# Kernel tuning notes

Hardware: AMD Instinct MI355X
Metric: run time of the kernel (lower is better)

Reference implementation:

```python
import jax, jax.numpy as jnp
import numpy as np

EPS = 1e-05


def layer_norm(x, a, b):
    m = jnp.mean(x, axis=-1, keepdims=True)
    v = jnp.var(x, axis=-1, keepdims=True)
    return a * (x - m) / jnp.sqrt(v + EPS) + b


def setup_inputs() -> dict:
    key = jax.random.key(0)
    ks = jax.random.split(key, 16)
    b, n, d, h = 1, 384, 128, 128
    s = 1.0 / np.sqrt(d)
    inp = {
        "x": jax.random.normal(ks[0], (b, n, n, d), dtype=jnp.float32),
        "norm_a": jnp.ones((d,), jnp.float32),
        "norm_b": jnp.zeros((d,), jnp.float32),
        "Wl": jax.random.normal(ks[1], (d, h), jnp.float32) * s,
        "bl": jnp.zeros((h,), jnp.float32),
        "Wr": jax.random.normal(ks[2], (d, h), jnp.float32) * s,
        "br": jnp.zeros((h,), jnp.float32),
        "Wlg": jax.random.normal(ks[3], (d, h), jnp.float32) * s,
        "blg": jnp.ones((h,), jnp.float32),
        "Wrg": jax.random.normal(ks[4], (d, h), jnp.float32) * s,
        "brg": jnp.ones((h,), jnp.float32),
        "Wog": jax.random.normal(ks[5], (d, h), jnp.float32) * s,
        "bog": jnp.ones((h,), jnp.float32),
        "on_a": jnp.ones((h,), jnp.float32),
        "on_b": jnp.zeros((h,), jnp.float32),
        "Wo": jax.random.normal(ks[6], (h, d), jnp.float32) * s,
        "bo": jnp.zeros((d,), jnp.float32),
    }
    return inp


def reference(x, norm_a, norm_b, Wl, bl, Wr, br, Wlg, blg, Wrg, brg, Wog, bog, on_a, on_b, Wo, bo):
    n = x.shape[1]
    xn = layer_norm(x, norm_a, norm_b)
    left = (xn @ Wl + bl) * jax.nn.sigmoid(xn @ Wlg + blg)
    right = (xn @ Wr + br) * jax.nn.sigmoid(xn @ Wrg + brg)
    out_gate = jax.nn.sigmoid(xn @ Wog + bog)
    # ingoing mix: out[b,i,j,d] = sum_k left[b,k,j,d] * right[b,k,i,d], in fp32
    out = jnp.einsum('bkjd,bkid->bijd', left.astype(jnp.float32), right.astype(jnp.float32)) / n
    out = out.astype(x.dtype)
    out = layer_norm(out, on_a, on_b) * out_gate
    return out @ Wo + bo
```

## Files before the change

kernel.cpp:

```cpp
#include <hip/hip_runtime.h>
#include <hip/hip_bf16.h>

#define NN 384
#define DD 128
#define MM (NN*NN)

typedef __attribute__((ext_vector_type(8))) short short8;
typedef __attribute__((ext_vector_type(4))) float f32x4;

__device__ __forceinline__ unsigned short f2bf(float f){
  unsigned u = __float_as_uint(f);
  u += 0x7fffu + ((u >> 16) & 1u);
  return (unsigned short)(u >> 16);
}
__device__ __forceinline__ float bf2f(unsigned short u){
  return __uint_as_float(((unsigned)u) << 16);
}
__device__ __forceinline__ float sigm(float x){
  return 1.0f / (1.0f + __expf(-x));
}
__device__ __forceinline__ unsigned cvtpk(float lo, float hi){
  unsigned r;
  asm("v_cvt_pk_bf16_f32 %0, %1, %2" : "=v"(r) : "v"(lo), "v"(hi));
  return r;
}
__device__ __forceinline__ f32x4 mfma16(short8 a, short8 b, f32x4 c){
  return __builtin_amdgcn_mfma_f32_16x16x32_bf16(a, b, c, 0, 0, 0);
}
__device__ __forceinline__ void gll16(const void* g, void* l){
  __builtin_amdgcn_global_load_lds(
      (const __attribute__((address_space(1))) unsigned int*)g,
      (__attribute__((address_space(3))) unsigned int*)l, 16, 0, 0);
}

__global__ void k_prep(const float* __restrict__ Wl, const float* __restrict__ Wlg,
                       const float* __restrict__ Wr, const float* __restrict__ Wrg,
                       const float* __restrict__ Wog, const float* __restrict__ Wo,
                       unsigned short* __restrict__ Wcat, unsigned short* __restrict__ Wot){
  int n = blockIdx.x;
  if(n < 640){
    const float* src; int col;
    if(n < 128){ src = Wl;  col = n; }
    else if(n < 256){ src = Wlg; col = n-128; }
    else if(n < 384){ src = Wr;  col = n-256; }
    else if(n < 512){ src = Wrg; col = n-384; }
    else            { src = Wog; col = n-512; }
    for(int k = threadIdx.x; k < 128; k += 64)
      Wcat[n*128 + k] = f2bf(src[k*128 + col]);
  } else {
    int c = n - 640;
    for(int k = threadIdx.x; k < 128; k += 64)
      Wot[c*128 + k] = f2bf(Wo[k*128 + c]);
  }
}

__global__ __launch_bounds__(256) void k_ln_x(const float* __restrict__ x,
    const float* __restrict__ na, const float* __restrict__ nb,
    unsigned short* __restrict__ xn){
  int wid = threadIdx.x >> 6, lane = threadIdx.x & 63;
  long r = (long)blockIdx.x*4 + wid;
  float2 v = *(const float2*)(x + r*DD + lane*2);
  float s  = v.x + v.y;
  float sq = v.x*v.x + v.y*v.y;
  #pragma unroll
  for(int m = 32; m >= 1; m >>= 1){ s += __shfl_xor(s, m); sq += __shfl_xor(sq, m); }
  float mean = s  * (1.0f/128.0f);
  float var  = sq * (1.0f/128.0f) - mean*mean;
  float rstd = rsqrtf(var + 1e-5f);
  float2 a = *(const float2*)(na + lane*2);
  float2 b = *(const float2*)(nb + lane*2);
  unsigned pk = (unsigned)f2bf(a.x*(v.x-mean)*rstd + b.x)
              | ((unsigned)f2bf(a.y*(v.y-mean)*rstd + b.y) << 16);
  *(unsigned*)(xn + r*DD + lane*2) = pk;
}

__global__ __launch_bounds__(256, 4) void k_proj(
    const unsigned short* __restrict__ xn, const unsigned short* __restrict__ Wcat,
    const float* __restrict__ bl, const float* __restrict__ blg,
    const float* __restrict__ br, const float* __restrict__ brg,
    unsigned short* __restrict__ Lt, unsigned short* __restrict__ Rt){
  __shared__ char lds[2][16384];
  const int tid = threadIdx.x;
  const int wid = tid >> 6, lane = tid & 63;
  const int lrow = lane & 15, lgrp = lane >> 4;
  const int b = blockIdx.x;
  const int f = b / 288;
  const int w = b % 288;

  const int ws = wid >> 1;
  const int wd = wid & 1;
  const int d  = f*32 + wd*16 + lrow;

  short8 bv[4], bg[4];
  #pragma unroll
  for(int ks = 0; ks < 4; ++ks){
    bv[ks] = *(const short8*)(Wcat + (ws*256 + d)*DD + ks*32 + lgrp*8);
    bg[ks] = *(const short8*)(Wcat + (ws*256 + 128 + d)*DD + ks*32 + lgrp*8);
  }
  const float b0v = (ws ? br  : bl )[d];
  const float b1v = (ws ? brg : blg)[d];
  const float sc  = ws ? 1.0f : (1.0f/384.0f);
  unsigned short* const base = (ws ? Rt : Lt) + (long)d*MM;

  auto stage = [&](int buf, int v){
    int j = v/6, kb = v%6;
    int rsub = lane >> 4, c = lane & 15;
    #pragma unroll
    for(int p = 0; p < 4; ++p){
      int r0 = p*16 + wid*4;
      int r = r0 + rsub;
      gll16(xn + ((long)(kb*64 + r)*NN + j)*DD + (c ^ (r & 7))*8, &lds[buf][r0*256]);
    }
  };

  stage(0, w*8);
  __syncthreads();
  int cur = 0;
  for(int i = 0; i < 8; ++i){
    int v = w*8 + i;
    if(i < 7) stage(cur^1, v+1);

    f32x4 zero = {0.f,0.f,0.f,0.f};
    f32x4 acc[4][2];
    #pragma unroll
    for(int a1=0;a1<4;++a1){ acc[a1][0] = zero; acc[a1][1] = zero; }

    #pragma unroll
    for(int ks = 0; ks < 4; ++ks){
      #pragma unroll
      for(int fr = 0; fr < 4; ++fr){
        int r = fr*16 + lrow;
        short8 af = *(const short8*)(&lds[cur][r*256 + (((ks*4+lgrp)*16) ^ ((r&7)<<4))]);
        acc[fr][0] = mfma16(af, bv[ks], acc[fr][0]);
        acc[fr][1] = mfma16(af, bg[ks], acc[fr][1]);
      }
    }

    int j = v/6, kb = v%6;
    unsigned short* dst = base + (long)j*NN + kb*64;
    #pragma unroll
    for(int fr = 0; fr < 4; ++fr){
      float v0 = (acc[fr][0][0] + b0v)*sigm(acc[fr][1][0] + b1v)*sc;
      float v1 = (acc[fr][0][1] + b0v)*sigm(acc[fr][1][1] + b1v)*sc;
      float v2 = (acc[fr][0][2] + b0v)*sigm(acc[fr][1][2] + b1v)*sc;
      float v3 = (acc[fr][0][3] + b0v)*sigm(acc[fr][1][3] + b1v)*sc;
      uint2 pk; pk.x = cvtpk(v0, v1); pk.y = cvtpk(v2, v3);
      *(uint2*)(dst + fr*16 + lgrp*4) = pk;
    }
    __syncthreads();
    cur ^= 1;
  }
}

__global__ __launch_bounds__(256) void k_einsum(
    const unsigned short* __restrict__ Rt, const unsigned short* __restrict__ Lt,
    unsigned short* __restrict__ mid){
  __shared__ char lds[65536];
  const int b = blockIdx.x;
  const int xcd = b & 7, slot = b >> 3;
  const int d = (slot/9)*8 + xcd;
  const int t = slot % 9;
  const int it = t/3, jt = t%3;
  const int i0 = it*128, j0 = jt*128;
  const unsigned short* Abase = Lt + (long)d*MM;
  const unsigned short* Bbase = Rt + (long)d*MM;
  const int wid = threadIdx.x >> 6, lane = threadIdx.x & 63;
  const int wr = wid >> 1, wc = wid & 1;
  const int lrow = lane & 15, lgrp = lane >> 4;

  auto stage = [&](int buf, int kt){
    int k = kt*64;
    int c = lane & 7;
    #pragma unroll
    for(int t8 = 0; t8 < 8; ++t8){
      int rr = wid*64 + t8*8 + (lane >> 3);
      int r = rr & 127;
      const unsigned short* src = (rr < 128) ? (Abase + (long)(j0+r)*NN + k)
                                             : (Bbase + (long)(i0+r)*NN + k);
      gll16(src + (c ^ (r & 7))*8, &lds[buf*32768 + (wid*64 + t8*8)*128]);
    }
  };

  f32x4 zero = {0.f,0.f,0.f,0.f};
  f32x4 acc[4][4];
  #pragma unroll
  for(int a1 = 0; a1 < 4; ++a1)
    #pragma unroll
    for(int a2 = 0; a2 < 4; ++a2) acc[a1][a2] = zero;

  stage(0, 0);
  __syncthreads();
  for(int kt = 0; kt < 6; ++kt){
    int cur = kt & 1;
    if(kt < 5) stage(cur ^ 1, kt + 1);
    const int base = cur*32768;
    #pragma unroll
    for(int ks = 0; ks < 2; ++ks){
      short8 af[4], bf[4];
      #pragma unroll
      for(int f = 0; f < 4; ++f){
        int rj = wr*64 + f*16 + lrow;
        af[f] = *(const short8*)(&lds[base + rj*128 + (((ks*4+lgrp)*16) ^ ((rj & 7) << 4))]);
        int ri = wc*64 + f*16 + lrow;
        bf[f] = *(const short8*)(&lds[base + 16384 + ri*128 + (((ks*4+lgrp)*16) ^ ((ri & 7) << 4))]);
      }
      #pragma unroll
      for(int fj = 0; fj < 4; ++fj)
        #pragma unroll
        for(int fi = 0; fi < 4; ++fi)
          acc[fj][fi] = mfma16(af[fj], bf[fi], acc[fj][fi]);
    }
    __syncthreads();
  }

  #pragma unroll
  for(int fj = 0; fj < 4; ++fj){
    int j = j0 + wr*64 + fj*16 + lgrp*4;
    #pragma unroll
    for(int fi = 0; fi < 4; ++fi){
      int i = i0 + wc*64 + fi*16 + lrow;
      uint2 pk;
      pk.x = cvtpk(acc[fj][fi][0], acc[fj][fi][1]);
      pk.y = cvtpk(acc[fj][fi][2], acc[fj][fi][3]);
      *(uint2*)(mid + (long)d*MM + (long)i*NN + j) = pk;
    }
  }
}

__global__ __launch_bounds__(256) void k_final(
    const unsigned short* __restrict__ mid, const unsigned short* __restrict__ xn,
    const unsigned short* __restrict__ Wcat,
    const float* __restrict__ bog,
    const float* __restrict__ ona, const float* __restrict__ onb,
    const unsigned short* __restrict__ Wot, const float* __restrict__ bo,
    float* __restrict__ out){
  __shared__ unsigned short midt[64][144];
  __shared__ char slds[16384];
  __shared__ char glds[16384];
  const int tid = threadIdx.x;
  const int wid = tid >> 6, lane = tid & 63;
  const int lrow = lane & 15, lgrp = lane >> 4;
  const int i = blockIdx.y;
  const int j0 = blockIdx.x*64;

  {
    int rsub = lane >> 4, c = lane & 15;
    #pragma unroll
    for(int p = 0; p < 4; ++p){
      int r0 = p*16 + wid*4;
      int r = r0 + rsub;
      gll16(xn + ((long)i*NN + j0 + r)*DD + (c ^ (r & 7))*8, &slds[r0*256]);
    }
  }
  const int wc = wid;
  short8 ag[2][4];
  #pragma unroll
  for(int cf = 0; cf < 2; ++cf)
    #pragma unroll
    for(int ks = 0; ks < 4; ++ks)
      ag[cf][ks] = *(const short8*)(Wcat + (512 + wc*32 + cf*16 + lrow)*DD + ks*32 + lgrp*8);

  {
    int jp = tid & 15, dr = tid >> 4;
    #pragma unroll
    for(int pass = 0; pass < 8; ++pass){
      int dd = pass*16 + dr;
      uint2 v = *(const uint2*)(mid + (long)dd*MM + (long)i*NN + j0 + jp*4);
      midt[jp*4+0][dd] = (unsigned short)(v.x & 0xffffu);
      midt[jp*4+1][dd] = (unsigned short)(v.x >> 16);
      midt[jp*4+2][dd] = (unsigned short)(v.y & 0xffffu);
      midt[jp*4+3][dd] = (unsigned short)(v.y >> 16);
    }
  }
  __syncthreads();

  {
    f32x4 zero = {0.f,0.f,0.f,0.f};
    f32x4 accg[2][4];
    #pragma unroll
    for(int a1=0;a1<2;++a1)
      #pragma unroll
      for(int a2=0;a2<4;++a2) accg[a1][a2] = zero;
    #pragma unroll
    for(int ks = 0; ks < 4; ++ks){
      short8 bx[4];
      #pragma unroll
      for(int mf = 0; mf < 4; ++mf){
        int r = mf*16 + lrow;
        bx[mf] = *(const short8*)(&slds[r*256 + (((ks*4+lgrp)*16) ^ ((r&7)<<4))]);
      }
      #pragma unroll
      for(int cf = 0; cf < 2; ++cf)
        #pragma unroll
        for(int mf = 0; mf < 4; ++mf)
          accg[cf][mf] = mfma16(ag[cf][ks], bx[mf], accg[cf][mf]);
    }
    #pragma unroll
    for(int cf = 0; cf < 2; ++cf){
      int c0 = wc*32 + cf*16 + lgrp*4;
      float4 b4 = *(const float4*)(bog + c0);
      #pragma unroll
      for(int mf = 0; mf < 4; ++mf){
        int rr = mf*16 + lrow;
        uint2 pk;
        pk.x = cvtpk(sigm(accg[cf][mf][0] + b4.x), sigm(accg[cf][mf][1] + b4.y));
        pk.y = cvtpk(sigm(accg[cf][mf][2] + b4.z), sigm(accg[cf][mf][3] + b4.w));
        *(uint2*)(&glds[rr*256 + ((c0*2) ^ ((rr&7)<<4))]) = pk;
      }
    }
  }
  __syncthreads();

  {
    int j = tid >> 2, s = tid & 3;
    float vals[32];
    float sum = 0.f, sq = 0.f;
    #pragma unroll
    for(int o8 = 0; o8 < 4; ++o8){
      short8 h = *(const short8*)(&midt[j][s*32 + o8*8]);
      #pragma unroll
      for(int q = 0; q < 8; ++q){
        float vq = bf2f((unsigned short)h[q]);
        vals[o8*8+q] = vq; sum += vq; sq += vq*vq;
      }
    }
    #pragma unroll
    for(int m = 1; m < 4; m <<= 1){ sum += __shfl_xor(sum, m); sq += __shfl_xor(sq, m); }
    float mean = sum*(1.f/128.f);
    float var  = sq *(1.f/128.f) - mean*mean;
    float rstd = rsqrtf(var + 1e-5f);
    #pragma unroll
    for(int o = 0; o < 32; o += 4){
      int dd = s*32 + o;
      uint2 gv = *(const uint2*)(&glds[j*256 + ((dd*2) ^ ((j&7)<<4))]);
      float g0 = bf2f((unsigned short)(gv.x & 0xffffu));
      float g1 = bf2f((unsigned short)(gv.x >> 16));
      float g2 = bf2f((unsigned short)(gv.y & 0xffffu));
      float g3 = bf2f((unsigned short)(gv.y >> 16));
      float4 a4 = *(const float4*)(ona + dd);
      float4 b4 = *(const float4*)(onb + dd);
      float v0 = (a4.x*(vals[o]  -mean)*rstd + b4.x)*g0;
      float v1 = (a4.y*(vals[o+1]-mean)*rstd + b4.y)*g1;
      float v2 = (a4.z*(vals[o+2]-mean)*rstd + b4.z)*g2;
      float v3 = (a4.w*(vals[o+3]-mean)*rstd + b4.w)*g3;
      uint2 pk; pk.x = cvtpk(v0, v1); pk.y = cvtpk(v2, v3);
      *(uint2*)(&slds[j*256 + ((dd*2) ^ ((j&7)<<4))]) = pk;
    }
  }
  __syncthreads();

  {
    f32x4 zero = {0.f,0.f,0.f,0.f};
    f32x4 acc[8];
    #pragma unroll
    for(int fc = 0; fc < 8; ++fc) acc[fc] = zero;
    #pragma unroll 1
    for(int ks = 0; ks < 4; ++ks){
      int row = wid*16 + lrow;
      short8 a = *(const short8*)(&slds[row*256 + (((ks*4+lgrp)*16) ^ ((row & 7) << 4))]);
      #pragma unroll
      for(int fc = 0; fc < 8; ++fc){
        int n = fc*16 + lrow;
        short8 bfr = *(const short8*)(Wot + n*DD + ks*32 + lgrp*8);
        acc[fc] = mfma16(a, bfr, acc[fc]);
      }
    }
    #pragma unroll
    for(int fc = 0; fc < 8; ++fc){
      int c = fc*16 + lrow;
      float bb = bo[c];
      #pragma unroll
      for(int q = 0; q < 4; ++q){
        int jl = wid*16 + lgrp*4 + q;
        out[((long)i*NN + j0 + jl)*DD + c] = acc[fc][q] + bb;
      }
    }
  }
}

extern "C" void kernel_launch(void* const* d_in, const int* in_sizes, int n_in,
                              void* d_out, int out_size, void* d_ws, size_t ws_size,
                              hipStream_t stream){
  const float* x   = (const float*)d_in[0];
  const float* na  = (const float*)d_in[1];
  const float* nb  = (const float*)d_in[2];
  const float* Wl  = (const float*)d_in[3];
  const float* bl  = (const float*)d_in[4];
  const float* Wr  = (const float*)d_in[5];
  const float* br  = (const float*)d_in[6];
  const float* Wlg = (const float*)d_in[7];
  const float* blg = (const float*)d_in[8];
  const float* Wrg = (const float*)d_in[9];
  const float* brg = (const float*)d_in[10];
  const float* Wog = (const float*)d_in[11];
  const float* bog = (const float*)d_in[12];
  const float* ona = (const float*)d_in[13];
  const float* onb = (const float*)d_in[14];
  const float* Wo  = (const float*)d_in[15];
  const float* bo  = (const float*)d_in[16];
  float* out = (float*)d_out;

  char* ws = (char*)d_ws;
  const size_t SZ = (size_t)MM*DD*2;
  unsigned short* xn   = (unsigned short*)(ws);
  unsigned short* Lt   = (unsigned short*)(ws + SZ);
  unsigned short* Rt   = (unsigned short*)(ws + 2*SZ);
  unsigned short* mid  = (unsigned short*)(ws + 3*SZ);
  unsigned short* Wcat = (unsigned short*)(ws + 4*SZ);
  unsigned short* Wot  = (unsigned short*)(ws + 4*SZ + (size_t)640*128*2);

  k_prep  <<<768, 64, 0, stream>>>(Wl, Wlg, Wr, Wrg, Wog, Wo, Wcat, Wot);
  k_ln_x  <<<MM/4, 256, 0, stream>>>(x, na, nb, xn);
  k_proj  <<<1152, 256, 0, stream>>>(xn, Wcat, bl, blg, br, brg, Lt, Rt);
  k_einsum<<<1152, 256, 0, stream>>>(Rt, Lt, mid);
  k_final <<<dim3(6, 384), 256, 0, stream>>>(mid, xn, Wcat, bog, ona, onb, Wot, bo, out);
}
```

Before: 197.2 us.

## Move output-gate GEMM into the layernorm kernel and slim k_final

Fuses the output-gate projection and sigmoid into the input layernorm kernel, which now keeps the normalized tile in LDS and writes a swizzled bf16 gate buffer. k_final no longer reloads xn or runs the gate GEMM. It just async-copies the precomputed gate tile into LDS and reuses that buffer for the normalized, gated activations, which cuts LDS use and allows a higher occupancy hint. The mid buffer now aliases xn to save workspace. The cost is an extra gate round-trip through global memory and a heavier first kernel.

```diff
diff --git a/kernel.cpp b/kernel.cpp
--- a/kernel.cpp
+++ b/kernel.cpp
@@ -54,24 +54,69 @@
   }
 }
 
-__global__ __launch_bounds__(256) void k_ln_x(const float* __restrict__ x,
-    const float* __restrict__ na, const float* __restrict__ nb,
-    unsigned short* __restrict__ xn){
-  int wid = threadIdx.x >> 6, lane = threadIdx.x & 63;
-  long r = (long)blockIdx.x*4 + wid;
-  float2 v = *(const float2*)(x + r*DD + lane*2);
-  float s  = v.x + v.y;
-  float sq = v.x*v.x + v.y*v.y;
-  #pragma unroll
-  for(int m = 32; m >= 1; m >>= 1){ s += __shfl_xor(s, m); sq += __shfl_xor(sq, m); }
-  float mean = s  * (1.0f/128.0f);
-  float var  = sq * (1.0f/128.0f) - mean*mean;
-  float rstd = rsqrtf(var + 1e-5f);
-  float2 a = *(const float2*)(na + lane*2);
-  float2 b = *(const float2*)(nb + lane*2);
-  unsigned pk = (unsigned)f2bf(a.x*(v.x-mean)*rstd + b.x)
-              | ((unsigned)f2bf(a.y*(v.y-mean)*rstd + b.y) << 16);
-  *(unsigned*)(xn + r*DD + lane*2) = pk;
+__global__ __launch_bounds__(256, 3) void k_lng(
+    const float* __restrict__ x, const float* __restrict__ na,
+    const float* __restrict__ nb, const unsigned short* __restrict__ Wcat,
+    const float* __restrict__ bog,
+    unsigned short* __restrict__ xn, unsigned short* __restrict__ gate){
+  __shared__ char lds[32768];
+  const int tid = threadIdx.x;
+  const int wid = tid >> 6, lane = tid & 63;
+  const int lrow = lane & 15, lgrp = lane >> 4;
+  const long m0 = (long)blockIdx.x * 128;
+
+  float2 a2 = *(const float2*)(na + lane*2);
+  float2 b2 = *(const float2*)(nb + lane*2);
+
+  #pragma unroll 2
+  for(int it = 0; it < 32; ++it){
+    int r = wid*32 + it;
+    float2 v = *(const float2*)(x + (m0 + r)*DD + lane*2);
+    float s = v.x + v.y, sq = v.x*v.x + v.y*v.y;
+    #pragma unroll
+    for(int m = 32; m >= 1; m >>= 1){ s += __shfl_xor(s,m); sq += __shfl_xor(sq,m); }
+    float mean = s*(1.f/128.f);
+    float var  = sq*(1.f/128.f) - mean*mean;
+    float rstd = rsqrtf(var + 1e-5f);
+    unsigned pk = cvtpk(a2.x*(v.x-mean)*rstd + b2.x,
+                        a2.y*(v.y-mean)*rstd + b2.y);
+    *(unsigned*)(xn + (m0+r)*DD + lane*2) = pk;
+    *(unsigned*)(&lds[r*256 + ((lane*4) ^ ((r&7)<<4))]) = pk;
+  }
+  __syncthreads();
+
+  f32x4 acc[2][8];
+  #pragma unroll
+  for(int cf = 0; cf < 2; ++cf){
+    int c0 = wid*32 + cf*16 + lgrp*4;
+    float4 b4 = *(const float4*)(bog + c0);
+    #pragma unroll
+    for(int mf = 0; mf < 8; ++mf) acc[cf][mf] = (f32x4){b4.x,b4.y,b4.z,b4.w};
+  }
+  #pragma unroll
+  for(int ks = 0; ks < 4; ++ks){
+    short8 af0 = *(const short8*)(Wcat + (512 + wid*32 + lrow)*DD + ks*32 + lgrp*8);
+    short8 af1 = *(const short8*)(Wcat + (512 + wid*32 + 16 + lrow)*DD + ks*32 + lgrp*8);
+    #pragma unroll
+    for(int mf = 0; mf < 8; ++mf){
+      int r = mf*16 + lrow;
+      short8 bx = *(const short8*)(&lds[r*256 + (((ks*4+lgrp)*16) ^ ((r&7)<<4))]);
+      acc[0][mf] = mfma16(af0, bx, acc[0][mf]);
+      acc[1][mf] = mfma16(af1, bx, acc[1][mf]);
+    }
+  }
+  #pragma unroll
+  for(int cf = 0; cf < 2; ++cf){
+    int c0 = wid*32 + cf*16 + lgrp*4;
+    #pragma unroll
+    for(int mf = 0; mf < 8; ++mf){
+      int rr = mf*16 + lrow;
+      uint2 pk;
+      pk.x = cvtpk(sigm(acc[cf][mf][0]), sigm(acc[cf][mf][1]));
+      pk.y = cvtpk(sigm(acc[cf][mf][2]), sigm(acc[cf][mf][3]));
+      *(uint2*)((char*)gate + (m0+rr)*256 + ((c0*2) ^ ((rr&7)<<4))) = pk;
+    }
+  }
 }
 
 __global__ __launch_bounds__(256, 4) void k_proj(
@@ -227,16 +272,13 @@
   }
 }
 
-__global__ __launch_bounds__(256) void k_final(
-    const unsigned short* __restrict__ mid, const unsigned short* __restrict__ xn,
-    const unsigned short* __restrict__ Wcat,
-    const float* __restrict__ bog,
+__global__ __launch_bounds__(256, 4) void k_final(
+    const unsigned short* __restrict__ mid, const unsigned short* __restrict__ gate,
     const float* __restrict__ ona, const float* __restrict__ onb,
     const unsigned short* __restrict__ Wot, const float* __restrict__ bo,
     float* __restrict__ out){
-  __shared__ unsigned short midt[64][144];
-  __shared__ char slds[16384];
-  __shared__ char glds[16384];
+  __shared__ unsigned short midt[64][136];
+  __shared__ char gv[16384];
   const int tid = threadIdx.x;
   const int wid = tid >> 6, lane = tid & 63;
   const int lrow = lane & 15, lgrp = lane >> 4;
@@ -244,22 +286,11 @@
   const int j0 = blockIdx.x*64;
 
   {
-    int rsub = lane >> 4, c = lane & 15;
-    #pragma unroll
-    for(int p = 0; p < 4; ++p){
-      int r0 = p*16 + wid*4;
-      int r = r0 + rsub;
-      gll16(xn + ((long)i*NN + j0 + r)*DD + (c ^ (r & 7))*8, &slds[r0*256]);
-    }
-  }
-  const int wc = wid;
-  short8 ag[2][4];
-  #pragma unroll
-  for(int cf = 0; cf < 2; ++cf)
-    #pragma unroll
-    for(int ks = 0; ks < 4; ++ks)
-      ag[cf][ks] = *(const short8*)(Wcat + (512 + wc*32 + cf*16 + lrow)*DD + ks*32 + lgrp*8);
-
+    const char* gsrc = (const char*)gate + ((long)i*NN + j0)*256;
+    #pragma unroll
+    for(int p = 0; p < 4; ++p)
+      gll16(gsrc + p*4096 + wid*1024 + lane*16, &gv[p*4096 + wid*1024]);
+  }
   {
     int jp = tid & 15, dr = tid >> 4;
     #pragma unroll
@@ -275,43 +306,6 @@
   __syncthreads();
 
   {
-    f32x4 zero = {0.f,0.f,0.f,0.f};
-    f32x4 accg[2][4];
-    #pragma unroll
-    for(int a1=0;a1<2;++a1)
-      #pragma unroll
-      for(int a2=0;a2<4;++a2) accg[a1][a2] = zero;
-    #pragma unroll
-    for(int ks = 0; ks < 4; ++ks){
-      short8 bx[4];
-      #pragma unroll
-      for(int mf = 0; mf < 4; ++mf){
-        int r = mf*16 + lrow;
-        bx[mf] = *(const short8*)(&slds[r*256 + (((ks*4+lgrp)*16) ^ ((r&7)<<4))]);
-      }
-      #pragma unroll
-      for(int cf = 0; cf < 2; ++cf)
-        #pragma unroll
-        for(int mf = 0; mf < 4; ++mf)
-          accg[cf][mf] = mfma16(ag[cf][ks], bx[mf], accg[cf][mf]);
-    }
-    #pragma unroll
-    for(int cf = 0; cf < 2; ++cf){
-      int c0 = wc*32 + cf*16 + lgrp*4;
-      float4 b4 = *(const float4*)(bog + c0);
-      #pragma unroll
-      for(int mf = 0; mf < 4; ++mf){
-        int rr = mf*16 + lrow;
-        uint2 pk;
-        pk.x = cvtpk(sigm(accg[cf][mf][0] + b4.x), sigm(accg[cf][mf][1] + b4.y));
-        pk.y = cvtpk(sigm(accg[cf][mf][2] + b4.z), sigm(accg[cf][mf][3] + b4.w));
-        *(uint2*)(&glds[rr*256 + ((c0*2) ^ ((rr&7)<<4))]) = pk;
-      }
-    }
-  }
-  __syncthreads();
-
-  {
     int j = tid >> 2, s = tid & 3;
     float vals[32];
     float sum = 0.f, sq = 0.f;
@@ -332,11 +326,12 @@
     #pragma unroll
     for(int o = 0; o < 32; o += 4){
       int dd = s*32 + o;
-      uint2 gv = *(const uint2*)(&glds[j*256 + ((dd*2) ^ ((j&7)<<4))]);
-      float g0 = bf2f((unsigned short)(gv.x & 0xffffu));
-      float g1 = bf2f((unsigned short)(gv.x >> 16));
-      float g2 = bf2f((unsigned short)(gv.y & 0xffffu));
-      float g3 = bf2f((unsigned short)(gv.y >> 16));
+      char* gp = &gv[j*256 + ((dd*2) ^ ((j&7)<<4))];
+      uint2 gvv = *(uint2*)gp;
+      float g0 = bf2f((unsigned short)(gvv.x & 0xffffu));
+      float g1 = bf2f((unsigned short)(gvv.x >> 16));
+      float g2 = bf2f((unsigned short)(gvv.y & 0xffffu));
+      float g3 = bf2f((unsigned short)(gvv.y >> 16));
       float4 a4 = *(const float4*)(ona + dd);
       float4 b4 = *(const float4*)(onb + dd);
       float v0 = (a4.x*(vals[o]  -mean)*rstd + b4.x)*g0;
@@ -344,7 +339,7 @@
       float v2 = (a4.z*(vals[o+2]-mean)*rstd + b4.z)*g2;
       float v3 = (a4.w*(vals[o+3]-mean)*rstd + b4.w)*g3;
       uint2 pk; pk.x = cvtpk(v0, v1); pk.y = cvtpk(v2, v3);
-      *(uint2*)(&slds[j*256 + ((dd*2) ^ ((j&7)<<4))]) = pk;
+      *(uint2*)gp = pk;
     }
   }
   __syncthreads();
@@ -357,11 +352,10 @@
     #pragma unroll 1
     for(int ks = 0; ks < 4; ++ks){
       int row = wid*16 + lrow;
-      short8 a = *(const short8*)(&slds[row*256 + (((ks*4+lgrp)*16) ^ ((row & 7) << 4))]);
+      short8 a = *(const short8*)(&gv[row*256 + (((ks*4+lgrp)*16) ^ ((row & 7) << 4))]);
       #pragma unroll
       for(int fc = 0; fc < 8; ++fc){
-        int n = fc*16 + lrow;
-        short8 bfr = *(const short8*)(Wot + n*DD + ks*32 + lgrp*8);
+        short8 bfr = *(const short8*)(Wot + (fc*16 + lrow)*DD + ks*32 + lgrp*8);
         acc[fc] = mfma16(a, bfr, acc[fc]);
       }
     }
@@ -405,13 +399,14 @@
   unsigned short* xn   = (unsigned short*)(ws);
   unsigned short* Lt   = (unsigned short*)(ws + SZ);
   unsigned short* Rt   = (unsigned short*)(ws + 2*SZ);
-  unsigned short* mid  = (unsigned short*)(ws + 3*SZ);
+  unsigned short* gate = (unsigned short*)(ws + 3*SZ);
   unsigned short* Wcat = (unsigned short*)(ws + 4*SZ);
   unsigned short* Wot  = (unsigned short*)(ws + 4*SZ + (size_t)640*128*2);
+  unsigned short* mid  = xn;
 
   k_prep  <<<768, 64, 0, stream>>>(Wl, Wlg, Wr, Wrg, Wog, Wo, Wcat, Wot);
-  k_ln_x  <<<MM/4, 256, 0, stream>>>(x, na, nb, xn);
+  k_lng   <<<1152, 256, 0, stream>>>(x, na, nb, Wcat, bog, xn, gate);
   k_proj  <<<1152, 256, 0, stream>>>(xn, Wcat, bl, blg, br, brg, Lt, Rt);
   k_einsum<<<1152, 256, 0, stream>>>(Rt, Lt, mid);
-  k_final <<<dim3(6, 384), 256, 0, stream>>>(mid, xn, Wcat, bog, ona, onb, Wot, bo, out);
-}
+  k_final <<<dim3(6, 384), 256, 0, stream>>>(mid, gate, ona, onb, Wot, bo, out);
+}
```

New measurement: 211.4 us. 7.2% more time.
